# Performance work log

Measured on AMD Instinct MI355X. Metric: run time of the kernel, lower is better.

The kernel has to match this reference:

```python
import jax, jax.numpy as jnp
import numpy as np

B, C, H, W = 4, 256, 56, 56
K = 7
STRIDE = 1
DIL = 1
GROUPS = 16          # channels // group_channels(16)
GC = C // GROUPS     # 16 channels per group
PAD = (K + (K - 1) * (DIL - 1) - 1) // 2  # = 3
BN_EPS = 1e-5


def setup_inputs() -> dict:
    key = jax.random.key(0)
    ks = jax.random.split(key, 3)
    x = jax.random.normal(ks[0], (B, C, H, W), dtype=jnp.float32)
    # conv1: 1x1, C -> C//4, no bias (followed by BN)
    w1 = jax.random.normal(ks[1], (C // 4, C), dtype=jnp.float32) * (1.0 / np.sqrt(C))
    bn_gamma = jnp.ones((C // 4,), jnp.float32)
    bn_beta = jnp.zeros((C // 4,), jnp.float32)
    bn_mean = jnp.zeros((C // 4,), jnp.float32)
    bn_var = jnp.ones((C // 4,), jnp.float32)
    # conv2: 1x1, C//4 -> K*K*groups, with bias
    w2 = jax.random.normal(ks[2], (K * K * GROUPS, C // 4), dtype=jnp.float32) * (1.0 / np.sqrt(C // 4))
    b2 = jnp.zeros((K * K * GROUPS,), jnp.float32)
    return {"x": x, "w1": w1, "bn_gamma": bn_gamma, "bn_beta": bn_beta,
            "bn_mean": bn_mean, "bn_var": bn_var, "w2": w2, "b2": b2}


def _gen_weight(x, w1, bn_gamma, bn_beta, bn_mean, bn_var, w2, b2):
    # conv1 (1x1) + BN (inference stats) + ReLU
    h = jnp.einsum('oc,bchw->bohw', w1, x)
    scale = bn_gamma / jnp.sqrt(bn_var + BN_EPS)
    h = h * scale[None, :, None, None] + (bn_beta - bn_mean * scale)[None, :, None, None]
    h = jax.nn.relu(h)
    # conv2 (1x1) -> [B, K*K*groups, H, W]
    w = jnp.einsum('oc,bchw->bohw', w2, h) + b2[None, :, None, None]
    return w.reshape(B, GROUPS, K, K, H, W)


def _involution(x, weight):
    # x: [B,C,H,W], weight: [B,G,K,K,Ho,Wo]; stride=1 so Ho=H, Wo=W
    xp = jnp.pad(x, ((0, 0), (0, 0), (PAD, PAD), (PAD, PAD)))
    # gather K*K shifted views -> [B, C, K*K, H, W]
    patches = jnp.stack(
        [xp[:, :, i * DIL:i * DIL + H, j * DIL:j * DIL + W]
         for i in range(K) for j in range(K)], axis=2)
    patches = patches.reshape(B, GROUPS, GC, K * K, H, W)
    wflat = weight.reshape(B, GROUPS, K * K, H, W)
    out = jnp.einsum('bgckhw,bgkhw->bgchw', patches, wflat)
    return out.reshape(B, C, H, W)


def reference(x, w1, bn_gamma, bn_beta, bn_mean, bn_var, w2, b2):
    weight = _gen_weight(x, w1, bn_gamma, bn_beta, bn_mean, bn_var, w2, b2)
    return _involution(x, weight)
```

## Files before the change

kernel.cpp:

```cpp
#include <hip/hip_runtime.h>

typedef __attribute__((ext_vector_type(8))) short short8;
typedef __attribute__((ext_vector_type(4))) float f32x4;
typedef __attribute__((ext_vector_type(4))) unsigned int u32x4;
typedef unsigned short ushort_t;

#define BB 4
#define HW 3136
#define NX (4*256*3136)
#define LDS_W2P 14336
#define LDS_B2S 29696
#define LDS_TOT 29952

#define K1_XB0 32768
#define K1_XB1 36864
#define K1_BIAS 40960
#define K1_TOT 41216

__device__ __forceinline__ unsigned int f2bf(float f) {
    unsigned int u = __float_as_uint(f);
    return (u + 0x7FFFu + ((u >> 16) & 1u)) >> 16;
}

__global__ void k0_prep(const float* __restrict__ w1, const float* __restrict__ gamma,
                        const float* __restrict__ beta, const float* __restrict__ mean,
                        const float* __restrict__ var, ushort_t* __restrict__ w1bf,
                        float* __restrict__ bias_d) {
    int idx = blockIdx.x * 256 + threadIdx.x;
    int o = idx >> 8;
    float sc = gamma[o] * rsqrtf(var[o] + 1e-5f);
    w1bf[idx] = (ushort_t)f2bf(w1[idx] * sc);
    if (idx < 64)
        bias_d[idx] = beta[idx] - mean[idx] * (gamma[idx] * rsqrtf(var[idx] + 1e-5f));
}

__global__ __launch_bounds__(256) void k1_mfma(
        const float* __restrict__ x, const ushort_t* __restrict__ w1bf,
        const float* __restrict__ bias_d, ushort_t* __restrict__ h_g) {
    __shared__ __align__(16) char lds[K1_TOT];
    int blk = blockIdx.x;
    int tile = blk % 56, b = blk / 56;
    int px0 = tile * 56;
    int tid = threadIdx.x;
    int lane = tid & 63, w = tid >> 6;

    for (int i = tid; i < 2048; i += 256) {
        int row = i >> 5, col = (i & 31) << 4;
        u32x4 v = *(const u32x4*)(w1bf + i * 8);
        *(u32x4*)(lds + (row << 9) + (col ^ ((row & 7) << 4))) = v;
    }
    if (tid < 64) ((float*)(lds + K1_BIAS))[tid] = bias_d[tid];

    int spx = tid & 63, scg = tid >> 6;
    int gpx = min(px0 + spx, HW - 1);
    const float* xbase = x + (size_t)b * 256 * HW + gpx;
    int sdst_off = spx * 64 + ((scg << 4) ^ ((spx & 3) << 4));

    float xr[8];
#pragma unroll
    for (int u = 0; u < 8; u++) xr[u] = xbase[(size_t)(scg * 8 + u) * HW];

    f32x4 acc[4];
#pragma unroll
    for (int n = 0; n < 4; n++) acc[n] = (f32x4){0.f, 0.f, 0.f, 0.f};

    {
        unsigned int pk[4];
#pragma unroll
        for (int j = 0; j < 4; j++)
            pk[j] = f2bf(xr[2 * j]) | (f2bf(xr[2 * j + 1]) << 16);
        u32x4 v = {pk[0], pk[1], pk[2], pk[3]};
        *(u32x4*)(lds + K1_XB0 + sdst_off) = v;
    }
    __syncthreads();

    int arow = w * 16 + (lane & 15);
    int a_off = arow * 64 + (((lane >> 4) << 4) ^ ((arow & 3) << 4));

    for (int ks = 0; ks < 8; ks++) {
        if (ks < 7) {
            const float* xp = xbase + (size_t)((ks + 1) * 32 + scg * 8) * HW;
#pragma unroll
            for (int u = 0; u < 8; u++) xr[u] = xp[(size_t)u * HW];
        }
        int xb = (ks & 1) ? K1_XB1 : K1_XB0;
        short8 a = *(const short8*)(lds + xb + a_off);
#pragma unroll
        for (int n = 0; n < 4; n++) {
            int brow = n * 16 + (lane & 15);
            short8 bb = *(const short8*)(lds + (brow << 9) +
                          ((ks * 64 + ((lane >> 4) << 4)) ^ ((brow & 7) << 4)));
            acc[n] = __builtin_amdgcn_mfma_f32_16x16x32_bf16(a, bb, acc[n], 0, 0, 0);
        }
        __syncthreads();
        if (ks < 7) {
            unsigned int pk[4];
#pragma unroll
            for (int j = 0; j < 4; j++)
                pk[j] = f2bf(xr[2 * j]) | (f2bf(xr[2 * j + 1]) << 16);
            u32x4 v = {pk[0], pk[1], pk[2], pk[3]};
            *(u32x4*)(lds + ((ks & 1) ? K1_XB0 : K1_XB1) + sdst_off) = v;
            __syncthreads();
        }
    }

#pragma unroll
    for (int n = 0; n < 4; n++) {
        int o = n * 16 + (lane & 15);
        float bo = ((const float*)(lds + K1_BIAS))[o];
#pragma unroll
        for (int r = 0; r < 4; r++) {
            int pxl = w * 16 + ((lane >> 4) << 2) + r;
            if (pxl < 56) {
                float v = fmaxf(acc[n][r] + bo, 0.f);
                h_g[((size_t)b * HW + px0 + pxl) * 64 + o] = (ushort_t)f2bf(v);
            }
        }
    }
}

__global__ __launch_bounds__(256, 5) void k2_fused(
        const float* __restrict__ x, const ushort_t* __restrict__ h_g,
        const float* __restrict__ w2, const float* __restrict__ b2,
        float* __restrict__ out) {
    __shared__ __align__(16) char lds[LDS_TOT];
    int wid = blockIdx.x;
    int xcd = wid & 7, pos = wid >> 3;
    int work = xcd * 224 + pos;
    int b = work / 448;
    int r0 = work % 448;
    int tchunk = r0 >> 6, r2 = r0 & 63;
    int g = r2 >> 2;
    int tile = (tchunk << 2) + (r2 & 3);
    int tid = threadIdx.x;

    const char* hg = (const char*)h_g + ((size_t)b * HW + tile * 112) * 128;
    for (int i = tid; i < 896; i += 256) {
        int row = i >> 3, cb = (i & 7) << 4;
        u32x4 v = *(const u32x4*)(hg + row * 128 + cb);
        *(u32x4*)(lds + row * 128 + (cb ^ ((row & 7) << 4))) = v;
    }
    {
        int k = tid >> 2, cg = tid & 3;
        unsigned int pk[8];
        if (k < 49) {
            const float* wr = w2 + ((size_t)(g * 49 + k)) * 64 + cg * 16;
#pragma unroll
            for (int i = 0; i < 8; i++)
                pk[i] = f2bf(wr[2 * i]) | (f2bf(wr[2 * i + 1]) << 16);
        } else {
#pragma unroll
            for (int i = 0; i < 8; i++) pk[i] = 0;
        }
#pragma unroll
        for (int hh = 0; hh < 2; hh++) {
            u32x4 v = {pk[hh * 4 + 0], pk[hh * 4 + 1], pk[hh * 4 + 2], pk[hh * 4 + 3]};
            *(u32x4*)(lds + LDS_W2P + k * 128 + ((cg * 32 + hh * 16) ^ ((k & 7) << 4))) = v;
        }
    }
    if (tid < 49) ((float*)(lds + LDS_B2S))[tid] = b2[g * 49 + tid];
    __syncthreads();

    int lane = tid & 63, wd = tid >> 6;
    f32x4 acc[7];
#pragma unroll
    for (int n = 0; n < 7; n++) acc[n] = (f32x4){0.f, 0.f, 0.f, 0.f};
    int arow = wd * 16 + (lane & 15);
#pragma unroll
    for (int ks = 0; ks < 2; ks++) {
        int kc = ks * 64 + ((lane >> 4) << 4);
        short8 a = *(const short8*)(lds + LDS_W2P + arow * 128 + (kc ^ ((arow & 7) << 4)));
#pragma unroll
        for (int n = 0; n < 7; n++) {
            int brow = n * 16 + (lane & 15);
            short8 bb = *(const short8*)(lds + brow * 128 + (kc ^ ((brow & 7) << 4)));
            acc[n] = __builtin_amdgcn_mfma_f32_16x16x32_bf16(a, bb, acc[n], 0, 0, 0);
        }
    }
    __syncthreads();

    {
        const float* b2s = (const float*)(lds + LDS_B2S);
#pragma unroll
        for (int n = 0; n < 7; n++) {
#pragma unroll
            for (int rr = 0; rr < 4; rr++) {
                int tap = wd * 16 + ((lane >> 4) << 2) + rr;
                if (tap < 49) {
                    int px = n * 16 + (lane & 15);
                    ((float*)lds)[tap * 116 + px] = acc[n][rr] + b2s[tap];
                }
            }
        }
    }
    __syncthreads();

    int cq = tid >> 5, pg = tid & 31;
    if (pg < 28) {
        int py = (pg >= 14) ? 1 : 0;
        int x0 = (pg - 14 * py) * 4;
        int c0 = g * 16 + cq * 2;
        int rowb = tile * 2 + py;
        float accd[2][4] = {{0.f, 0.f, 0.f, 0.f}, {0.f, 0.f, 0.f, 0.f}};
        for (int ky = 0; ky < 7; ky++) {
            int rr = rowb + ky - 3;
            if (rr < 0 || rr >= 56) continue;
            float w[2][12];
#pragma unroll
            for (int cc = 0; cc < 2; cc++) {
                int base = (b * 256 + c0 + cc) * HW + rr * 56 + x0 - 4;
#pragma unroll
                for (int k3 = 0; k3 < 3; k3++) {
                    int o = base + k3 * 4;
                    o = min(max(o, 0), NX - 4);
                    *(f32x4*)&w[cc][k3 * 4] = *(const f32x4*)(x + o);
                }
            }
            if (x0 == 0) {
                w[0][1] = w[0][2] = w[0][3] = 0.f;
                w[1][1] = w[1][2] = w[1][3] = 0.f;
            }
            if (x0 == 52) {
                w[0][8] = w[0][9] = w[0][10] = 0.f;
                w[1][8] = w[1][9] = w[1][10] = 0.f;
            }
#pragma unroll
            for (int kx = 0; kx < 7; kx++) {
                f32x4 wg = *(const f32x4*)(lds + ((ky * 7 + kx) * 116 + py * 56 + x0) * 4);
#pragma unroll
                for (int cc = 0; cc < 2; cc++) {
#pragma unroll
                    for (int pi = 0; pi < 4; pi++)
                        accd[cc][pi] = fmaf(wg[pi], w[cc][pi + kx + 1], accd[cc][pi]);
                }
            }
        }
#pragma unroll
        for (int cc = 0; cc < 2; cc++) {
            f32x4 st = {accd[cc][0], accd[cc][1], accd[cc][2], accd[cc][3]};
            *(f32x4*)(out + (size_t)(b * 256 + c0 + cc) * HW + tile * 112 + pg * 4) = st;
        }
    }
}

extern "C" void kernel_launch(void* const* d_in, const int* in_sizes, int n_in,
                              void* d_out, int out_size, void* d_ws, size_t ws_size,
                              hipStream_t stream) {
    const float* x     = (const float*)d_in[0];
    const float* w1    = (const float*)d_in[1];
    const float* gamma = (const float*)d_in[2];
    const float* beta  = (const float*)d_in[3];
    const float* mean  = (const float*)d_in[4];
    const float* var   = (const float*)d_in[5];
    const float* w2    = (const float*)d_in[6];
    const float* b2    = (const float*)d_in[7];
    float* out = (float*)d_out;

    ushort_t* w1bf  = (ushort_t*)d_ws;
    float* bias_d   = (float*)((char*)d_ws + 32768);
    ushort_t* h_g   = (ushort_t*)((char*)d_ws + 36864);

    k0_prep<<<64, 256, 0, stream>>>(w1, gamma, beta, mean, var, w1bf, bias_d);
    k1_mfma<<<224, 256, 0, stream>>>(x, w1bf, bias_d, h_g);
    k2_fused<<<1792, 256, 0, stream>>>(x, h_g, w2, b2, out);
}
```

Measured before the change: 39.77 us.

## Fold BN prep into conv1 kernel and double k2 tile with bf16 weight staging

Removes the separate prep kernel: k1 now computes the BN scale and bias itself and converts w1 to bf16 directly into LDS, saving one launch. k2 processes 4 rows (224 pixels) per block instead of 2, halving the grid so the w2 staging and x halo loads are amortised over more work. Generated involution weights are stored in LDS as bf16 to fit the larger tile, and each thread computes 8 outputs per channel. In exchange, more registers are used and occupancy is lowered (launch bounds drop from 5 to 4), and the bf16 rounding of the generated weights adds precision loss.

```diff
diff --git a/kernel.cpp b/kernel.cpp
--- a/kernel.cpp
+++ b/kernel.cpp
@@ -8,35 +8,27 @@
 #define BB 4
 #define HW 3136
 #define NX (4*256*3136)
-#define LDS_W2P 14336
-#define LDS_B2S 29696
-#define LDS_TOT 29952
 
 #define K1_XB0 32768
 #define K1_XB1 36864
 #define K1_BIAS 40960
-#define K1_TOT 41216
+#define K1_SCV 41216
+#define K1_TOT 41472
+
+#define K2_W2P 28672
+#define K2_B2S 36864
+#define K2_TOT 37120
 
 __device__ __forceinline__ unsigned int f2bf(float f) {
     unsigned int u = __float_as_uint(f);
     return (u + 0x7FFFu + ((u >> 16) & 1u)) >> 16;
 }
 
-__global__ void k0_prep(const float* __restrict__ w1, const float* __restrict__ gamma,
-                        const float* __restrict__ beta, const float* __restrict__ mean,
-                        const float* __restrict__ var, ushort_t* __restrict__ w1bf,
-                        float* __restrict__ bias_d) {
-    int idx = blockIdx.x * 256 + threadIdx.x;
-    int o = idx >> 8;
-    float sc = gamma[o] * rsqrtf(var[o] + 1e-5f);
-    w1bf[idx] = (ushort_t)f2bf(w1[idx] * sc);
-    if (idx < 64)
-        bias_d[idx] = beta[idx] - mean[idx] * (gamma[idx] * rsqrtf(var[idx] + 1e-5f));
-}
-
 __global__ __launch_bounds__(256) void k1_mfma(
-        const float* __restrict__ x, const ushort_t* __restrict__ w1bf,
-        const float* __restrict__ bias_d, ushort_t* __restrict__ h_g) {
+        const float* __restrict__ x, const float* __restrict__ w1,
+        const float* __restrict__ gamma, const float* __restrict__ beta,
+        const float* __restrict__ mean, const float* __restrict__ var,
+        ushort_t* __restrict__ h_g) {
     __shared__ __align__(16) char lds[K1_TOT];
     int blk = blockIdx.x;
     int tile = blk % 56, b = blk / 56;
@@ -44,13 +36,6 @@
     int tid = threadIdx.x;
     int lane = tid & 63, w = tid >> 6;
 
-    for (int i = tid; i < 2048; i += 256) {
-        int row = i >> 5, col = (i & 31) << 4;
-        u32x4 v = *(const u32x4*)(w1bf + i * 8);
-        *(u32x4*)(lds + (row << 9) + (col ^ ((row & 7) << 4))) = v;
-    }
-    if (tid < 64) ((float*)(lds + K1_BIAS))[tid] = bias_d[tid];
-
     int spx = tid & 63, scg = tid >> 6;
     int gpx = min(px0 + spx, HW - 1);
     const float* xbase = x + (size_t)b * 256 * HW + gpx;
@@ -59,6 +44,28 @@
     float xr[8];
 #pragma unroll
     for (int u = 0; u < 8; u++) xr[u] = xbase[(size_t)(scg * 8 + u) * HW];
+
+    if (tid < 64) {
+        float sc = gamma[tid] * rsqrtf(var[tid] + 1e-5f);
+        ((float*)(lds + K1_SCV))[tid] = sc;
+        ((float*)(lds + K1_BIAS))[tid] = beta[tid] - mean[tid] * sc;
+    }
+    __syncthreads();
+
+    for (int i = tid; i < 2048; i += 256) {
+        int row = i >> 5, col8 = i & 31;
+        const float* src = w1 + row * 256 + col8 * 8;
+        f32x4 a = *(const f32x4*)src;
+        f32x4 c = *(const f32x4*)(src + 4);
+        float sc = ((const float*)(lds + K1_SCV))[row];
+        unsigned int pk[4];
+        pk[0] = f2bf(a[0] * sc) | (f2bf(a[1] * sc) << 16);
+        pk[1] = f2bf(a[2] * sc) | (f2bf(a[3] * sc) << 16);
+        pk[2] = f2bf(c[0] * sc) | (f2bf(c[1] * sc) << 16);
+        pk[3] = f2bf(c[2] * sc) | (f2bf(c[3] * sc) << 16);
+        u32x4 v = {pk[0], pk[1], pk[2], pk[3]};
+        *(u32x4*)(lds + (row << 9) + ((col8 << 4) ^ ((row & 7) << 4))) = v;
+    }
 
     f32x4 acc[4];
 #pragma unroll
@@ -119,23 +126,23 @@
     }
 }
 
-__global__ __launch_bounds__(256, 5) void k2_fused(
+__global__ __launch_bounds__(256, 4) void k2_fused(
         const float* __restrict__ x, const ushort_t* __restrict__ h_g,
         const float* __restrict__ w2, const float* __restrict__ b2,
         float* __restrict__ out) {
-    __shared__ __align__(16) char lds[LDS_TOT];
-    int wid = blockIdx.x;
-    int xcd = wid & 7, pos = wid >> 3;
-    int work = xcd * 224 + pos;
-    int b = work / 448;
-    int r0 = work % 448;
-    int tchunk = r0 >> 6, r2 = r0 & 63;
-    int g = r2 >> 2;
-    int tile = (tchunk << 2) + (r2 & 3);
+    __shared__ __align__(16) char lds[K2_TOT];
+    int wid0 = blockIdx.x;
+    int xcd = wid0 & 7, pos = wid0 >> 3;
+    int work = xcd * 112 + pos;
+    int b = work / 224;
+    int rem = work - b * 224;
+    int half = rem / 112, r2 = rem - half * 112;
+    int tloc = r2 >> 4, g = r2 & 15;
+    int tile = half * 7 + tloc;
     int tid = threadIdx.x;
 
-    const char* hg = (const char*)h_g + ((size_t)b * HW + tile * 112) * 128;
-    for (int i = tid; i < 896; i += 256) {
+    const char* hg = (const char*)h_g + ((size_t)b * HW + tile * 224) * 128;
+    for (int i = tid; i < 1792; i += 256) {
         int row = i >> 3, cb = (i & 7) << 4;
         u32x4 v = *(const u32x4*)(hg + row * 128 + cb);
         *(u32x4*)(lds + row * 128 + (cb ^ ((row & 7) << 4))) = v;
@@ -155,23 +162,23 @@
 #pragma unroll
         for (int hh = 0; hh < 2; hh++) {
             u32x4 v = {pk[hh * 4 + 0], pk[hh * 4 + 1], pk[hh * 4 + 2], pk[hh * 4 + 3]};
-            *(u32x4*)(lds + LDS_W2P + k * 128 + ((cg * 32 + hh * 16) ^ ((k & 7) << 4))) = v;
-        }
-    }
-    if (tid < 49) ((float*)(lds + LDS_B2S))[tid] = b2[g * 49 + tid];
+            *(u32x4*)(lds + K2_W2P + k * 128 + ((cg * 32 + hh * 16) ^ ((k & 7) << 4))) = v;
+        }
+    }
+    if (tid < 49) ((float*)(lds + K2_B2S))[tid] = b2[g * 49 + tid];
     __syncthreads();
 
     int lane = tid & 63, wd = tid >> 6;
-    f32x4 acc[7];
-#pragma unroll
-    for (int n = 0; n < 7; n++) acc[n] = (f32x4){0.f, 0.f, 0.f, 0.f};
+    f32x4 acc[14];
+#pragma unroll
+    for (int n = 0; n < 14; n++) acc[n] = (f32x4){0.f, 0.f, 0.f, 0.f};
     int arow = wd * 16 + (lane & 15);
 #pragma unroll
     for (int ks = 0; ks < 2; ks++) {
         int kc = ks * 64 + ((lane >> 4) << 4);
-        short8 a = *(const short8*)(lds + LDS_W2P + arow * 128 + (kc ^ ((arow & 7) << 4)));
-#pragma unroll
-        for (int n = 0; n < 7; n++) {
+        short8 a = *(const short8*)(lds + K2_W2P + arow * 128 + (kc ^ ((arow & 7) << 4)));
+#pragma unroll
+        for (int n = 0; n < 14; n++) {
             int brow = n * 16 + (lane & 15);
             short8 bb = *(const short8*)(lds + brow * 128 + (kc ^ ((brow & 7) << 4)));
             acc[n] = __builtin_amdgcn_mfma_f32_16x16x32_bf16(a, bb, acc[n], 0, 0, 0);
@@ -180,65 +187,78 @@
     __syncthreads();
 
     {
-        const float* b2s = (const float*)(lds + LDS_B2S);
-#pragma unroll
-        for (int n = 0; n < 7; n++) {
+        const float* b2s = (const float*)(lds + K2_B2S);
+        ushort_t* wl = (ushort_t*)lds;
+#pragma unroll
+        for (int n = 0; n < 14; n++) {
 #pragma unroll
             for (int rr = 0; rr < 4; rr++) {
                 int tap = wd * 16 + ((lane >> 4) << 2) + rr;
                 if (tap < 49) {
                     int px = n * 16 + (lane & 15);
-                    ((float*)lds)[tap * 116 + px] = acc[n][rr] + b2s[tap];
+                    wl[tap * 232 + px] = (ushort_t)f2bf(acc[n][rr] + b2s[tap]);
                 }
             }
         }
     }
     __syncthreads();
 
-    int cq = tid >> 5, pg = tid & 31;
-    if (pg < 28) {
-        int py = (pg >= 14) ? 1 : 0;
-        int x0 = (pg - 14 * py) * 4;
-        int c0 = g * 16 + cq * 2;
-        int rowb = tile * 2 + py;
-        float accd[2][4] = {{0.f, 0.f, 0.f, 0.f}, {0.f, 0.f, 0.f, 0.f}};
+    int cpk = tid >> 5;
+    int pg = tid & 31;
+    int py = pg >> 3, xi = pg & 7;
+    if (xi < 7) {
+        int x0 = xi * 8;
+        int c0 = g * 16 + cpk * 2;
+        int rowb = tile * 4 + py;
+        float accd[2][8];
+#pragma unroll
+        for (int cc = 0; cc < 2; cc++)
+#pragma unroll
+            for (int pi = 0; pi < 8; pi++) accd[cc][pi] = 0.f;
+
         for (int ky = 0; ky < 7; ky++) {
             int rr = rowb + ky - 3;
             if (rr < 0 || rr >= 56) continue;
-            float w[2][12];
+            float w[2][16];
 #pragma unroll
             for (int cc = 0; cc < 2; cc++) {
                 int base = (b * 256 + c0 + cc) * HW + rr * 56 + x0 - 4;
 #pragma unroll
-                for (int k3 = 0; k3 < 3; k3++) {
-                    int o = base + k3 * 4;
+                for (int k4 = 0; k4 < 4; k4++) {
+                    int o = base + k4 * 4;
                     o = min(max(o, 0), NX - 4);
-                    *(f32x4*)&w[cc][k3 * 4] = *(const f32x4*)(x + o);
+                    *(f32x4*)&w[cc][k4 * 4] = *(const f32x4*)(x + o);
                 }
             }
             if (x0 == 0) {
-                w[0][1] = w[0][2] = w[0][3] = 0.f;
-                w[1][1] = w[1][2] = w[1][3] = 0.f;
-            }
-            if (x0 == 52) {
-                w[0][8] = w[0][9] = w[0][10] = 0.f;
-                w[1][8] = w[1][9] = w[1][10] = 0.f;
+#pragma unroll
+                for (int cc = 0; cc < 2; cc++) { w[cc][1] = w[cc][2] = w[cc][3] = 0.f; }
+            }
+            if (x0 == 48) {
+#pragma unroll
+                for (int cc = 0; cc < 2; cc++) { w[cc][12] = w[cc][13] = w[cc][14] = 0.f; }
             }
 #pragma unroll
             for (int kx = 0; kx < 7; kx++) {
-                f32x4 wg = *(const f32x4*)(lds + ((ky * 7 + kx) * 116 + py * 56 + x0) * 4);
-#pragma unroll
-                for (int cc = 0; cc < 2; cc++) {
-#pragma unroll
-                    for (int pi = 0; pi < 4; pi++)
-                        accd[cc][pi] = fmaf(wg[pi], w[cc][pi + kx + 1], accd[cc][pi]);
+                u32x4 wv = *(const u32x4*)(lds + ((ky * 7 + kx) * 232 + py * 56 + x0) * 2);
+                float wf[8];
+#pragma unroll
+                for (int j = 0; j < 4; j++) {
+                    wf[2 * j]     = __uint_as_float(wv[j] << 16);
+                    wf[2 * j + 1] = __uint_as_float(wv[j] & 0xFFFF0000u);
                 }
+#pragma unroll
+                for (int cc = 0; cc < 2; cc++)
+#pragma unroll
+                    for (int pi = 0; pi < 8; pi++)
+                        accd[cc][pi] = fmaf(wf[pi], w[cc][pi + kx + 1], accd[cc][pi]);
             }
         }
 #pragma unroll
         for (int cc = 0; cc < 2; cc++) {
-            f32x4 st = {accd[cc][0], accd[cc][1], accd[cc][2], accd[cc][3]};
-            *(f32x4*)(out + (size_t)(b * 256 + c0 + cc) * HW + tile * 112 + pg * 4) = st;
+            float* op = out + (size_t)(b * 256 + c0 + cc) * HW + tile * 224 + py * 56 + x0;
+            *(f32x4*)op = (f32x4){accd[cc][0], accd[cc][1], accd[cc][2], accd[cc][3]};
+            *(f32x4*)(op + 4) = (f32x4){accd[cc][4], accd[cc][5], accd[cc][6], accd[cc][7]};
         }
     }
 }
@@ -256,11 +276,8 @@
     const float* b2    = (const float*)d_in[7];
     float* out = (float*)d_out;
 
-    ushort_t* w1bf  = (ushort_t*)d_ws;
-    float* bias_d   = (float*)((char*)d_ws + 32768);
-    ushort_t* h_g   = (ushort_t*)((char*)d_ws + 36864);
-
-    k0_prep<<<64, 256, 0, stream>>>(w1, gamma, beta, mean, var, w1bf, bias_d);
-    k1_mfma<<<224, 256, 0, stream>>>(x, w1bf, bias_d, h_g);
-    k2_fused<<<1792, 256, 0, stream>>>(x, h_g, w2, b2, out);
-}
+    ushort_t* h_g = (ushort_t*)d_ws;
+
+    k1_mfma<<<224, 256, 0, stream>>>(x, w1, gamma, beta, mean, var, h_g);
+    k2_fused<<<896, 256, 0, stream>>>(x, h_g, w2, b2, out);
+}
```

Result: faster. 35.00 us (-12.0%).
